# Optimization experiments

Hardware: AMD Instinct MI355X
Metric: run time of the kernel (lower is better)

The kernel has to match this reference:

```python
import jax, jax.numpy as jnp
import numpy as np

D_MODEL = 1024
N_HEAD = 16
D_HEAD = D_MODEL // N_HEAD


def setup_inputs() -> dict:
    key = jax.random.key(0)
    k_x, k_qkv, k_proj = jax.random.split(key, 3)
    B, T = 2, 2048
    x = jax.random.normal(k_x, (B, T, D_MODEL), dtype=jnp.float32)
    # torch Linear weight [out, in]; y = x @ W.T. Scale ~ kaiming-uniform-ish.
    s = 1.0 / np.sqrt(D_MODEL)
    W_qkv = jax.random.uniform(k_qkv, (3 * D_MODEL, D_MODEL), dtype=jnp.float32, minval=-s, maxval=s)
    W_proj = jax.random.uniform(k_proj, (D_MODEL, D_MODEL), dtype=jnp.float32, minval=-s, maxval=s)
    return {"x": x, "W_qkv": W_qkv, "W_proj": W_proj}


def reference(x, W_qkv, W_proj):
    B, T, C = x.shape
    qkv = jnp.einsum('btc,oc->bto', x, W_qkv)  # [B,T,3C]
    q, k, v = jnp.split(qkv, 3, axis=-1)
    # [B,T,C] -> [B,H,T,Dh]
    def heads(t):
        return t.reshape(B, T, N_HEAD, D_HEAD).transpose(0, 2, 1, 3)
    q, k, v = heads(q), heads(k), heads(v)
    scale = 1.0 / np.sqrt(D_HEAD)
    scores = jnp.einsum('bhqd,bhkd->bhqk', q, k) * scale  # [B,H,T,T]
    causal = jnp.tril(jnp.ones((T, T), dtype=bool))
    scores = jnp.where(causal, scores, jnp.finfo(scores.dtype).min)
    attn = jax.nn.softmax(scores, axis=-1)
    y = jnp.einsum('bhqk,bhkd->bhqd', attn, v)  # [B,H,T,Dh]
    y = y.transpose(0, 2, 1, 3).reshape(B, T, C)
    return jnp.einsum('btc,oc->bto', y, W_proj)
```

## Files before the change

kernel.cpp:

```cpp
#include <hip/hip_runtime.h>

typedef unsigned short u16;
typedef float f32x4 __attribute__((ext_vector_type(4)));
typedef __bf16 bf16x8 __attribute__((ext_vector_type(8)));
typedef unsigned int u32x4 __attribute__((ext_vector_type(4)));
typedef u16 u16x4 __attribute__((ext_vector_type(4)));
typedef u16 u16x8 __attribute__((ext_vector_type(8)));

static __device__ __forceinline__ u16 f2bf(float f) {
  union { __bf16 h; u16 u; } c;
  c.h = (__bf16)f;
  return c.u;
}

static __device__ __forceinline__ void gload_lds16(const void* g, void* l) {
  __builtin_amdgcn_global_load_lds(
      (const __attribute__((address_space(1))) unsigned int*)g,
      (__attribute__((address_space(3))) unsigned int*)l, 16, 0, 0);
}

__global__ __launch_bounds__(256) void cvt3_f32_bf16(const float* __restrict__ a,
                                                     const float* __restrict__ bb,
                                                     const float* __restrict__ cc,
                                                     u16* __restrict__ out,
                                                     int n1, int n2, int n3) {
  int i = blockIdx.x * 256 + threadIdx.x;
  const float* src;
  int j = i;
  if (i < n1) { src = a; }
  else if (i < n1 + n2) { src = bb; j = i - n1; }
  else { src = cc; j = i - n1 - n2; if (j >= n3) return; }
  f32x4 v = *((const f32x4*)src + j);
  u16x4 o;
  o[0] = f2bf(v[0]); o[1] = f2bf(v[1]); o[2] = f2bf(v[2]); o[3] = f2bf(v[3]);
  *((u16x4*)out + i) = o;
}

template<int OUT_BF16, int FUSE_VT>
__global__ __launch_bounds__(256) void gemm_nt(const u16* __restrict__ A,
                                               const u16* __restrict__ B,
                                               void* __restrict__ Cp,
                                               u16* __restrict__ vt,
                                               int M, int N, int K, int gy) {
  __shared__ __align__(16) u16 lA[128 * 64];
  __shared__ __align__(16) u16 lB[128 * 64];
  const int tid = threadIdx.x;
  const int lane = tid & 63;
  const int wave = tid >> 6;
  const int wm = wave >> 1, wn = wave & 1;
  const int l15 = lane & 15, lg = lane >> 4;

  const int bid = blockIdx.x;
  const int xcd = bid & 7, s = bid >> 3;
  const int pnx = (N >> 7) >> 3;
  const int bm = (s % gy) * 128;
  const int bn = (xcd * pnx + s / gy) * 128;

  f32x4 acc[4][4];
#pragma unroll
  for (int i = 0; i < 4; ++i)
#pragma unroll
    for (int j = 0; j < 4; ++j) acc[i][j] = (f32x4){0.f, 0.f, 0.f, 0.f};

  const u16* Ag[4];
  const u16* Bg[4];
#pragma unroll
  for (int it = 0; it < 4; ++it) {
    const int ss = it * 256 + tid;
    const int row = ss >> 3, g = ss & 7;
    const int gsw = g ^ (row & 7);
    Ag[it] = A + (size_t)(bm + row) * K + gsw * 8;
    Bg[it] = B + (size_t)(bn + row) * K + gsw * 8;
  }

  for (int k0 = 0; k0 < K; k0 += 64) {
#pragma unroll
    for (int it = 0; it < 4; ++it) {
      gload_lds16(Ag[it] + k0, (u16*)lA + (size_t)(it * 256 + tid) * 8);
      gload_lds16(Bg[it] + k0, (u16*)lB + (size_t)(it * 256 + tid) * 8);
    }
    __syncthreads();
#pragma unroll
    for (int kk = 0; kk < 2; ++kk) {
      bf16x8 af[4], bfv[4];
#pragma unroll
      for (int mf = 0; mf < 4; ++mf) {
        const int row = wm * 64 + mf * 16 + l15;
        af[mf] = *(const bf16x8*)((const char*)lA + row * 128 +
                                  ((kk * 64 + lg * 16) ^ ((row & 7) << 4)));
      }
#pragma unroll
      for (int nf = 0; nf < 4; ++nf) {
        const int row = wn * 64 + nf * 16 + l15;
        bfv[nf] = *(const bf16x8*)((const char*)lB + row * 128 +
                                   ((kk * 64 + lg * 16) ^ ((row & 7) << 4)));
      }
#pragma unroll
      for (int mf = 0; mf < 4; ++mf)
#pragma unroll
        for (int nf = 0; nf < 4; ++nf)
          acc[mf][nf] = __builtin_amdgcn_mfma_f32_16x16x32_bf16(af[mf], bfv[nf], acc[mf][nf], 0, 0, 0);
    }
    __syncthreads();
  }

  if (FUSE_VT && bn >= 2048) {
#pragma unroll
    for (int mf = 0; mf < 4; ++mf) {
      const int row0 = bm + wm * 64 + mf * 16 + lg * 4;
      const int b = row0 >> 11, t0 = row0 & 2047;
#pragma unroll
      for (int nf = 0; nf < 4; ++nf) {
        const int colv = bn - 2048 + wn * 64 + nf * 16 + l15;
        const int h = colv >> 6, d = colv & 63;
        u16x4 pk;
        pk[0] = f2bf(acc[mf][nf][0]); pk[1] = f2bf(acc[mf][nf][1]);
        pk[2] = f2bf(acc[mf][nf][2]); pk[3] = f2bf(acc[mf][nf][3]);
        *(u16x4*)&vt[((size_t)((b * 16 + h) * 64 + d)) * 2048 + t0] = pk;
      }
    }
  } else {
#pragma unroll
    for (int mf = 0; mf < 4; ++mf) {
#pragma unroll
      for (int r = 0; r < 4; ++r) {
        const int row = bm + wm * 64 + mf * 16 + lg * 4 + r;
#pragma unroll
        for (int nf = 0; nf < 4; ++nf) {
          const int col = bn + wn * 64 + nf * 16 + l15;
          const float v = acc[mf][nf][r];
          if (OUT_BF16) ((u16*)Cp)[(size_t)row * N + col] = f2bf(v);
          else          ((float*)Cp)[(size_t)row * N + col] = v;
        }
      }
    }
  }
}

__global__ __launch_bounds__(256) void attn_fwd(const u16* __restrict__ qkv,
                                                const u16* __restrict__ vt,
                                                u16* __restrict__ y) {
  constexpr int T = 2048, C = 1024, C3 = 3072, D = 64, NQ = 32;
  __shared__ __align__(16) u16 lK[2][64 * 64];
  __shared__ __align__(16) u16 lV[3][64 * 64];
  __shared__ __align__(16) u16 lP[4 * 16 * 64];
  const int tid = threadIdx.x, lane = tid & 63, w = tid >> 6;
  const int l15 = lane & 15, lg = lane >> 4;

  const int bid = blockIdx.x;
  const int xcd = bid & 7, slot = bid >> 3;
  const int bh = xcd * 4 + (slot >> 4);
  const int pi = slot & 15;
  const int b = bh >> 4, h = bh & 15;

  const int r0 = tid >> 3, off0 = (tid & 7) * 8;
  const int r1 = (tid + 256) >> 3;
  const int sb0 = (off0 * 2) ^ ((r0 & 7) << 4);
  const int sb1 = (off0 * 2) ^ ((r1 & 7) << 4);
  const u16* Kbase = qkv + (size_t)b * T * C3 + C + h * D;
  const u16* Vbase = vt + (size_t)bh * D * T;

  const float qscale = 0.125f * 1.44269504088896f;

#pragma unroll 1
  for (int qi = 0; qi < 2; ++qi) {
    const int qt = (qi == 0) ? pi : (NQ - 1 - pi);
    const int q0 = qt * 64;

    const size_t qoff = ((size_t)b * T + q0 + w * 16 + l15) * C3 + h * D;
    const bf16x8 aq0 = *(const bf16x8*)&qkv[qoff + lg * 8];
    const bf16x8 aq1 = *(const bf16x8*)&qkv[qoff + 32 + lg * 8];

    float m = -1.0e30f, l = 0.f;
    f32x4 o_acc[4];
#pragma unroll
    for (int nf = 0; nf < 4; ++nf) o_acc[nf] = (f32x4){0.f, 0.f, 0.f, 0.f};

    u32x4 rk0 = *(const u32x4*)(Kbase + (size_t)r0 * C3 + off0);
    u32x4 rk1 = *(const u32x4*)(Kbase + (size_t)r1 * C3 + off0);
    u32x4 rv0 = *(const u32x4*)(Vbase + (size_t)r0 * T + off0);
    u32x4 rv1 = *(const u32x4*)(Vbase + (size_t)r1 * T + off0);
    __syncthreads();
    *(u32x4*)&lK[0][(r0 * 128 + sb0) >> 1] = rk0;
    *(u32x4*)&lK[0][(r1 * 128 + sb1) >> 1] = rk1;
    *(u32x4*)&lV[0][(r0 * 128 + sb0) >> 1] = rv0;
    *(u32x4*)&lV[0][(r1 * 128 + sb1) >> 1] = rv1;
    if (qt >= 1) {
      rk0 = *(const u32x4*)(Kbase + (size_t)(64 + r0) * C3 + off0);
      rk1 = *(const u32x4*)(Kbase + (size_t)(64 + r1) * C3 + off0);
      rv0 = *(const u32x4*)(Vbase + (size_t)r0 * T + 64 + off0);
      rv1 = *(const u32x4*)(Vbase + (size_t)r1 * T + 64 + off0);
    }

    int vcur = 0;
    for (int i = 0; i <= qt + 1; ++i) {
      const int vnext = (vcur == 2) ? 0 : vcur + 1;
      const int vprev = (vcur == 0) ? 2 : vcur - 1;
      __syncthreads();
      const int wr = i + 1;
      if (wr <= qt) {
        *(u32x4*)&lK[wr & 1][(r0 * 128 + sb0) >> 1] = rk0;
        *(u32x4*)&lK[wr & 1][(r1 * 128 + sb1) >> 1] = rk1;
        *(u32x4*)&lV[vnext][(r0 * 128 + sb0) >> 1] = rv0;
        *(u32x4*)&lV[vnext][(r1 * 128 + sb1) >> 1] = rv1;
        if (wr + 1 <= qt) {
          const int kn = (wr + 1) * 64;
          rk0 = *(const u32x4*)(Kbase + (size_t)(kn + r0) * C3 + off0);
          rk1 = *(const u32x4*)(Kbase + (size_t)(kn + r1) * C3 + off0);
          rv0 = *(const u32x4*)(Vbase + (size_t)r0 * T + kn + off0);
          rv1 = *(const u32x4*)(Vbase + (size_t)r1 * T + kn + off0);
        }
      }

      f32x4 s[4];
      if (i <= qt) {
        const u16* Kc = lK[i & 1];
#pragma unroll
        for (int nf = 0; nf < 4; ++nf) s[nf] = (f32x4){0.f, 0.f, 0.f, 0.f};
        __builtin_amdgcn_s_setprio(1);
#pragma unroll
        for (int nf = 0; nf < 4; ++nf) {
          const int row = nf * 16 + l15;
          const int x = (row & 7) << 4;
          bf16x8 bk0 = *(const bf16x8*)&Kc[(row * 128 + ((lg * 16) ^ x)) >> 1];
          bf16x8 bk1 = *(const bf16x8*)&Kc[(row * 128 + ((64 + lg * 16) ^ x)) >> 1];
          s[nf] = __builtin_amdgcn_mfma_f32_16x16x32_bf16(bk0, aq0, s[nf], 0, 0, 0);
          s[nf] = __builtin_amdgcn_mfma_f32_16x16x32_bf16(bk1, aq1, s[nf], 0, 0, 0);
        }
        __builtin_amdgcn_s_setprio(0);
      }

      if (i >= 1) {
        const u16* Vc = lV[vprev];
        __builtin_amdgcn_s_setprio(1);
#pragma unroll
        for (int sj = 0; sj < 2; ++sj) {
          bf16x8 ap = *(const bf16x8*)&lP[(w * 2048 + l15 * 128 + ((sj * 64 + lg * 16) ^ ((l15 & 7) << 4))) >> 1];
#pragma unroll
          for (int nf = 0; nf < 4; ++nf) {
            const int d = nf * 16 + l15;
            bf16x8 bv = *(const bf16x8*)&Vc[(d * 128 + ((sj * 64 + lg * 16) ^ ((d & 7) << 4))) >> 1];
            o_acc[nf] = __builtin_amdgcn_mfma_f32_16x16x32_bf16(ap, bv, o_acc[nf], 0, 0, 0);
          }
        }
        __builtin_amdgcn_s_setprio(0);
      }

      if (i <= qt) {
#pragma unroll
        for (int nf = 0; nf < 4; ++nf) {
#pragma unroll
          for (int r = 0; r < 4; ++r) {
            float v = s[nf][r] * qscale;
            if (i == qt) {
              if (nf * 16 + lg * 4 + r > w * 16 + l15) v = -1.0e30f;
            }
            s[nf][r] = v;
          }
        }

        float t0a = fmaxf(fmaxf(s[0][0], s[0][1]), fmaxf(s[0][2], s[0][3]));
        float t1a = fmaxf(fmaxf(s[1][0], s[1][1]), fmaxf(s[1][2], s[1][3]));
        float t2a = fmaxf(fmaxf(s[2][0], s[2][1]), fmaxf(s[2][2], s[2][3]));
        float t3a = fmaxf(fmaxf(s[3][0], s[3][1]), fmaxf(s[3][2], s[3][3]));
        float pmax = fmaxf(fmaxf(t0a, t1a), fmaxf(t2a, t3a));
        pmax = fmaxf(pmax, __shfl_xor(pmax, 16));
        pmax = fmaxf(pmax, __shfl_xor(pmax, 32));

        if (!__all(pmax <= m)) {
          const float mnew = fmaxf(m, pmax);
          const float fct = __builtin_amdgcn_exp2f(m - mnew);
          m = mnew;
          l *= fct;
#pragma unroll
          for (int r = 0; r < 4; ++r) {
            const float fr = __shfl(fct, lg * 4 + r);
#pragma unroll
            for (int nf = 0; nf < 4; ++nf) o_acc[nf][r] *= fr;
          }
        }

        float p[4][4];
#pragma unroll
        for (int nf = 0; nf < 4; ++nf)
#pragma unroll
          for (int r = 0; r < 4; ++r) p[nf][r] = __builtin_amdgcn_exp2f(s[nf][r] - m);
        float s0a = (p[0][0] + p[0][1]) + (p[0][2] + p[0][3]);
        float s1a = (p[1][0] + p[1][1]) + (p[1][2] + p[1][3]);
        float s2a = (p[2][0] + p[2][1]) + (p[2][2] + p[2][3]);
        float s3a = (p[3][0] + p[3][1]) + (p[3][2] + p[3][3]);
        float psum = (s0a + s1a) + (s2a + s3a);
        psum += __shfl_xor(psum, 16);
        psum += __shfl_xor(psum, 32);
        l += psum;

#pragma unroll
        for (int nf = 0; nf < 4; ++nf) {
          u16x4 pk;
          pk[0] = f2bf(p[nf][0]); pk[1] = f2bf(p[nf][1]);
          pk[2] = f2bf(p[nf][2]); pk[3] = f2bf(p[nf][3]);
          *(u16x4*)&lP[(w * 2048 + l15 * 128 + ((nf * 32 + lg * 8) ^ ((l15 & 7) << 4))) >> 1] = pk;
        }
      }

      vcur = vnext;
    }

#pragma unroll
    for (int r = 0; r < 4; ++r) {
      const float li = __builtin_amdgcn_rcpf(__shfl(l, lg * 4 + r));
      const int row = q0 + w * 16 + lg * 4 + r;
#pragma unroll
      for (int nf = 0; nf < 4; ++nf) {
        const int col = h * D + nf * 16 + l15;
        y[((size_t)b * T + row) * C + col] = f2bf(o_acc[nf][r] * li);
      }
    }
  }
}

extern "C" void kernel_launch(void* const* d_in, const int* in_sizes, int n_in,
                              void* d_out, int out_size, void* d_ws, size_t ws_size,
                              hipStream_t stream) {
  const float* x = (const float*)d_in[0];
  const float* Wqkv = (const float*)d_in[1];
  const float* Wproj = (const float*)d_in[2];
  float* out = (float*)d_out;

  constexpr int B = 2, T = 2048, C = 1024, C3 = 3072, H = 16, D = 64;
  constexpr int M = B * T;

  u16* xb = (u16*)d_ws;
  u16* wqkvb = xb + (size_t)M * C;
  u16* wprojb = wqkvb + (size_t)C3 * C;
  u16* qkvb = wprojb + (size_t)C * C;
  u16* vtb = qkvb + (size_t)M * C3;
  u16* yb = vtb + (size_t)M * C;

  constexpr int n1 = (M * C) / 4, n2 = (C3 * C) / 4, n3 = (C * C) / 4;
  cvt3_f32_bf16<<<dim3((n1 + n2 + n3 + 255) / 256), 256, 0, stream>>>(
      x, Wqkv, Wproj, xb, n1, n2, n3);

  gemm_nt<1, 1><<<dim3((C3 / 128) * (M / 128)), 256, 0, stream>>>(
      xb, wqkvb, qkvb, vtb, M, C3, C, M / 128);
  attn_fwd<<<dim3(512), 256, 0, stream>>>(qkvb, vtb, yb);
  gemm_nt<0, 0><<<dim3((C / 128) * (M / 128)), 256, 0, stream>>>(
      yb, wprojb, out, nullptr, M, C, C, M / 128);
}
```

Before: 114.5 us.

## Add 256x256 tiled QKV GEMM with direct-to-LDS loads and simplify attention pipeline

Adds a new gemm256 kernel with 256x256 output tiles, 512 threads and double-buffered global_load_lds staging, and uses it for the QKV projection instead of the 128x128 gemm_nt. The larger tile is meant to raise arithmetic intensity and cut global traffic. The attention kernel also drops its skewed software pipeline, where P·V lagged one K tile behind Q·K, in favour of a simple loop that computes QK, softmax and PV on the same tile with double buffers. This saves one V buffer but removes the overlap between the two matmuls. The grid is now 192 blocks, which may underfill 256 CUs.

```diff
diff --git a/kernel.cpp b/kernel.cpp
--- a/kernel.cpp
+++ b/kernel.cpp
@@ -137,12 +137,172 @@
   }
 }
 
+template<int OUT_BF16, int FUSE_VT>
+__global__ __launch_bounds__(512, 2) void gemm256(const u16* __restrict__ A,
+                                                  const u16* __restrict__ B,
+                                                  void* __restrict__ Cp,
+                                                  u16* __restrict__ vt,
+                                                  int M, int N, int K) {
+  __shared__ __align__(16) u16 shm[65536];
+  const int tid = threadIdx.x;
+  const int lane = tid & 63, wave = tid >> 6;
+  const int wm = wave >> 2, wn = wave & 3;
+  const int l15 = lane & 15, lg = lane >> 4;
+
+  const int bid = blockIdx.x;
+  const int g = (bid & 7) * ((int)gridDim.x >> 3) + (bid >> 3);
+  const int bm = (g & 15) * 256;
+  const int bn = (g >> 4) * 256;
+
+  size_t srcA[2][2], srcB[2][2];
+  int lo[2];
+#pragma unroll
+  for (int i = 0; i < 2; ++i) {
+    const int flat = i * 512 + tid;
+    const int row = flat >> 3, gg = flat & 7;
+    const int gsw = gg ^ (row & 7);
+    lo[i] = flat * 16;
+#pragma unroll
+    for (int half = 0; half < 2; ++half) {
+      srcA[i][half] = (size_t)(bm + half * 128 + row) * K + gsw * 8;
+      srcB[i][half] = (size_t)(bn + half * 128 + row) * K + gsw * 8;
+    }
+  }
+
+#define STAGE_A(buf, half, kt)                                                     \
+  do {                                                                             \
+    gload_lds16(A + srcA[0][half] + (size_t)(kt) * 64,                             \
+                (char*)shm + (buf) * 65536 + (half) * 16384 + lo[0]);              \
+    gload_lds16(A + srcA[1][half] + (size_t)(kt) * 64,                             \
+                (char*)shm + (buf) * 65536 + (half) * 16384 + lo[1]);              \
+  } while (0)
+#define STAGE_B(buf, half, kt)                                                     \
+  do {                                                                             \
+    gload_lds16(B + srcB[0][half] + (size_t)(kt) * 64,                             \
+                (char*)shm + (buf) * 65536 + 32768 + (half) * 16384 + lo[0]);      \
+    gload_lds16(B + srcB[1][half] + (size_t)(kt) * 64,                             \
+                (char*)shm + (buf) * 65536 + 32768 + (half) * 16384 + lo[1]);      \
+  } while (0)
+
+  f32x4 acc[8][4];
+#pragma unroll
+  for (int i = 0; i < 8; ++i)
+#pragma unroll
+    for (int j = 0; j < 4; ++j) acc[i][j] = (f32x4){0.f, 0.f, 0.f, 0.f};
+
+  STAGE_A(0, 0, 0); STAGE_A(0, 1, 0);
+  STAGE_B(0, 0, 0); STAGE_B(0, 1, 0);
+  STAGE_B(1, 0, 1); STAGE_B(1, 1, 1);
+  asm volatile("s_waitcnt vmcnt(4)" ::: "memory");
+  __builtin_amdgcn_s_barrier();
+  __builtin_amdgcn_sched_barrier(0);
+
+  const int NT2 = K / 128;
+#pragma unroll 1
+  for (int t = 0; t < NT2; ++t) {
+    const int k0 = 2 * t, k1 = 2 * t + 1;
+    const bool more = (t < NT2 - 1);
+
+#pragma unroll
+    for (int grp = 0; grp < 2; ++grp) {
+      const char* Ab = (char*)shm + grp * 65536;
+      const char* Bb = Ab + 32768;
+      bf16x8 bB[4][2];
+#pragma unroll
+      for (int j = 0; j < 4; ++j) {
+        if (j == 0) {
+#pragma unroll
+          for (int nn = 0; nn < 4; ++nn) {
+            const int r = wn * 64 + nn * 16 + l15;
+            const int x = (r & 7) << 4;
+            bB[nn][0] = *(const bf16x8*)(Bb + r * 128 + ((lg * 16) ^ x));
+            bB[nn][1] = *(const bf16x8*)(Bb + r * 128 + ((64 + lg * 16) ^ x));
+          }
+        }
+        bf16x8 af[2][2];
+#pragma unroll
+        for (int mm = 0; mm < 2; ++mm) {
+          const int r = wm * 128 + (2 * j + mm) * 16 + l15;
+          const int x = (r & 7) << 4;
+          af[mm][0] = *(const bf16x8*)(Ab + r * 128 + ((lg * 16) ^ x));
+          af[mm][1] = *(const bf16x8*)(Ab + r * 128 + ((64 + lg * 16) ^ x));
+        }
+        if (grp == 0) {
+          if (j == 0) { STAGE_A(1, 0, k1); }
+          if (j == 1) { STAGE_A(1, 1, k1); if (more) STAGE_B(0, 0, k0 + 2); }
+          if (j == 2) { if (more) STAGE_B(0, 1, k0 + 2); }
+        } else {
+          if (j == 0) { if (more) STAGE_A(0, 0, k0 + 2); }
+          if (j == 1) { if (more) { STAGE_A(0, 1, k0 + 2); STAGE_B(1, 0, k1 + 2); } }
+          if (j == 2) { if (more) STAGE_B(1, 1, k1 + 2); }
+        }
+        __builtin_amdgcn_s_barrier();
+        __builtin_amdgcn_s_setprio(1);
+#pragma unroll
+        for (int mm = 0; mm < 2; ++mm)
+#pragma unroll
+          for (int nn = 0; nn < 4; ++nn) {
+            acc[2 * j + mm][nn] = __builtin_amdgcn_mfma_f32_16x16x32_bf16(
+                af[mm][0], bB[nn][0], acc[2 * j + mm][nn], 0, 0, 0);
+            acc[2 * j + mm][nn] = __builtin_amdgcn_mfma_f32_16x16x32_bf16(
+                af[mm][1], bB[nn][1], acc[2 * j + mm][nn], 0, 0, 0);
+          }
+        __builtin_amdgcn_s_setprio(0);
+        if (j == 3) {
+          if (grp == 0) {
+            if (more) asm volatile("s_waitcnt vmcnt(4)" ::: "memory");
+            else      asm volatile("s_waitcnt vmcnt(0)" ::: "memory");
+          } else if (more) {
+            asm volatile("s_waitcnt vmcnt(4)" ::: "memory");
+          }
+        }
+        __builtin_amdgcn_s_barrier();
+        if (j == 3) __builtin_amdgcn_sched_barrier(0);
+      }
+    }
+  }
+#undef STAGE_A
+#undef STAGE_B
+
+  if (FUSE_VT && bn >= 2048) {
+#pragma unroll
+    for (int m = 0; m < 8; ++m) {
+      const int row0 = bm + wm * 128 + m * 16 + lg * 4;
+      const int b = row0 >> 11, t0 = row0 & 2047;
+#pragma unroll
+      for (int nn = 0; nn < 4; ++nn) {
+        const int colv = bn - 2048 + wn * 64 + nn * 16 + l15;
+        const int h = colv >> 6, d = colv & 63;
+        u16x4 pk;
+        pk[0] = f2bf(acc[m][nn][0]); pk[1] = f2bf(acc[m][nn][1]);
+        pk[2] = f2bf(acc[m][nn][2]); pk[3] = f2bf(acc[m][nn][3]);
+        *(u16x4*)&vt[((size_t)((b * 16 + h) * 64 + d)) * 2048 + t0] = pk;
+      }
+    }
+  } else {
+#pragma unroll
+    for (int m = 0; m < 8; ++m) {
+#pragma unroll
+      for (int r = 0; r < 4; ++r) {
+        const int row = bm + wm * 128 + m * 16 + lg * 4 + r;
+#pragma unroll
+        for (int nn = 0; nn < 4; ++nn) {
+          const int col = bn + wn * 64 + nn * 16 + l15;
+          const float v = acc[m][nn][r];
+          if (OUT_BF16) ((u16*)Cp)[(size_t)row * N + col] = f2bf(v);
+          else          ((float*)Cp)[(size_t)row * N + col] = v;
+        }
+      }
+    }
+  }
+}
+
 __global__ __launch_bounds__(256) void attn_fwd(const u16* __restrict__ qkv,
                                                 const u16* __restrict__ vt,
                                                 u16* __restrict__ y) {
   constexpr int T = 2048, C = 1024, C3 = 3072, D = 64, NQ = 32;
   __shared__ __align__(16) u16 lK[2][64 * 64];
-  __shared__ __align__(16) u16 lV[3][64 * 64];
+  __shared__ __align__(16) u16 lV[2][64 * 64];
   __shared__ __align__(16) u16 lP[4 * 16 * 64];
   const int tid = threadIdx.x, lane = tid & 63, w = tid >> 6;
   const int l15 = lane & 15, lg = lane >> 4;
@@ -185,125 +345,114 @@
     *(u32x4*)&lK[0][(r1 * 128 + sb1) >> 1] = rk1;
     *(u32x4*)&lV[0][(r0 * 128 + sb0) >> 1] = rv0;
     *(u32x4*)&lV[0][(r1 * 128 + sb1) >> 1] = rv1;
-    if (qt >= 1) {
+    if (qt > 0) {
       rk0 = *(const u32x4*)(Kbase + (size_t)(64 + r0) * C3 + off0);
       rk1 = *(const u32x4*)(Kbase + (size_t)(64 + r1) * C3 + off0);
       rv0 = *(const u32x4*)(Vbase + (size_t)r0 * T + 64 + off0);
       rv1 = *(const u32x4*)(Vbase + (size_t)r1 * T + 64 + off0);
     }
 
-    int vcur = 0;
-    for (int i = 0; i <= qt + 1; ++i) {
-      const int vnext = (vcur == 2) ? 0 : vcur + 1;
-      const int vprev = (vcur == 0) ? 2 : vcur - 1;
+    for (int kt = 0; kt <= qt; ++kt) {
+      const int cur = kt & 1;
       __syncthreads();
-      const int wr = i + 1;
-      if (wr <= qt) {
-        *(u32x4*)&lK[wr & 1][(r0 * 128 + sb0) >> 1] = rk0;
-        *(u32x4*)&lK[wr & 1][(r1 * 128 + sb1) >> 1] = rk1;
-        *(u32x4*)&lV[vnext][(r0 * 128 + sb0) >> 1] = rv0;
-        *(u32x4*)&lV[vnext][(r1 * 128 + sb1) >> 1] = rv1;
-        if (wr + 1 <= qt) {
-          const int kn = (wr + 1) * 64;
+      if (kt < qt) {
+        *(u32x4*)&lK[cur ^ 1][(r0 * 128 + sb0) >> 1] = rk0;
+        *(u32x4*)&lK[cur ^ 1][(r1 * 128 + sb1) >> 1] = rk1;
+        *(u32x4*)&lV[cur ^ 1][(r0 * 128 + sb0) >> 1] = rv0;
+        *(u32x4*)&lV[cur ^ 1][(r1 * 128 + sb1) >> 1] = rv1;
+        if (kt + 1 < qt) {
+          const int kn = (kt + 2) * 64;
           rk0 = *(const u32x4*)(Kbase + (size_t)(kn + r0) * C3 + off0);
           rk1 = *(const u32x4*)(Kbase + (size_t)(kn + r1) * C3 + off0);
           rv0 = *(const u32x4*)(Vbase + (size_t)r0 * T + kn + off0);
           rv1 = *(const u32x4*)(Vbase + (size_t)r1 * T + kn + off0);
         }
       }
+      const u16* Kc = lK[cur];
+      const u16* Vc = lV[cur];
 
       f32x4 s[4];
-      if (i <= qt) {
-        const u16* Kc = lK[i & 1];
-#pragma unroll
-        for (int nf = 0; nf < 4; ++nf) s[nf] = (f32x4){0.f, 0.f, 0.f, 0.f};
-        __builtin_amdgcn_s_setprio(1);
+#pragma unroll
+      for (int nf = 0; nf < 4; ++nf) s[nf] = (f32x4){0.f, 0.f, 0.f, 0.f};
+      __builtin_amdgcn_s_setprio(1);
+#pragma unroll
+      for (int nf = 0; nf < 4; ++nf) {
+        const int row = nf * 16 + l15;
+        const int x = (row & 7) << 4;
+        bf16x8 bk0 = *(const bf16x8*)&Kc[(row * 128 + ((lg * 16) ^ x)) >> 1];
+        bf16x8 bk1 = *(const bf16x8*)&Kc[(row * 128 + ((64 + lg * 16) ^ x)) >> 1];
+        s[nf] = __builtin_amdgcn_mfma_f32_16x16x32_bf16(bk0, aq0, s[nf], 0, 0, 0);
+        s[nf] = __builtin_amdgcn_mfma_f32_16x16x32_bf16(bk1, aq1, s[nf], 0, 0, 0);
+      }
+      __builtin_amdgcn_s_setprio(0);
+
+#pragma unroll
+      for (int nf = 0; nf < 4; ++nf) {
+#pragma unroll
+        for (int r = 0; r < 4; ++r) {
+          float v = s[nf][r] * qscale;
+          if (kt == qt) {
+            if (nf * 16 + lg * 4 + r > w * 16 + l15) v = -1.0e30f;
+          }
+          s[nf][r] = v;
+        }
+      }
+
+      float t0a = fmaxf(fmaxf(s[0][0], s[0][1]), fmaxf(s[0][2], s[0][3]));
+      float t1a = fmaxf(fmaxf(s[1][0], s[1][1]), fmaxf(s[1][2], s[1][3]));
+      float t2a = fmaxf(fmaxf(s[2][0], s[2][1]), fmaxf(s[2][2], s[2][3]));
+      float t3a = fmaxf(fmaxf(s[3][0], s[3][1]), fmaxf(s[3][2], s[3][3]));
+      float pmax = fmaxf(fmaxf(t0a, t1a), fmaxf(t2a, t3a));
+      pmax = fmaxf(pmax, __shfl_xor(pmax, 16));
+      pmax = fmaxf(pmax, __shfl_xor(pmax, 32));
+
+      if (!__all(pmax <= m)) {
+        const float mnew = fmaxf(m, pmax);
+        const float fct = __builtin_amdgcn_exp2f(m - mnew);
+        m = mnew;
+        l *= fct;
+#pragma unroll
+        for (int r = 0; r < 4; ++r) {
+          const float fr = __shfl(fct, lg * 4 + r);
+#pragma unroll
+          for (int nf = 0; nf < 4; ++nf) o_acc[nf][r] *= fr;
+        }
+      }
+
+      float p[4][4];
+#pragma unroll
+      for (int nf = 0; nf < 4; ++nf)
+#pragma unroll
+        for (int r = 0; r < 4; ++r) p[nf][r] = __builtin_amdgcn_exp2f(s[nf][r] - m);
+      float s0a = (p[0][0] + p[0][1]) + (p[0][2] + p[0][3]);
+      float s1a = (p[1][0] + p[1][1]) + (p[1][2] + p[1][3]);
+      float s2a = (p[2][0] + p[2][1]) + (p[2][2] + p[2][3]);
+      float s3a = (p[3][0] + p[3][1]) + (p[3][2] + p[3][3]);
+      float psum = (s0a + s1a) + (s2a + s3a);
+      psum += __shfl_xor(psum, 16);
+      psum += __shfl_xor(psum, 32);
+      l += psum;
+
+#pragma unroll
+      for (int nf = 0; nf < 4; ++nf) {
+        u16x4 pk;
+        pk[0] = f2bf(p[nf][0]); pk[1] = f2bf(p[nf][1]);
+        pk[2] = f2bf(p[nf][2]); pk[3] = f2bf(p[nf][3]);
+        *(u16x4*)&lP[(w * 2048 + l15 * 128 + ((nf * 32 + lg * 8) ^ ((l15 & 7) << 4))) >> 1] = pk;
+      }
+
+      __builtin_amdgcn_s_setprio(1);
+#pragma unroll
+      for (int sj = 0; sj < 2; ++sj) {
+        bf16x8 ap = *(const bf16x8*)&lP[(w * 2048 + l15 * 128 + ((sj * 64 + lg * 16) ^ ((l15 & 7) << 4))) >> 1];
 #pragma unroll
         for (int nf = 0; nf < 4; ++nf) {
-          const int row = nf * 16 + l15;
-          const int x = (row & 7) << 4;
-          bf16x8 bk0 = *(const bf16x8*)&Kc[(row * 128 + ((lg * 16) ^ x)) >> 1];
-          bf16x8 bk1 = *(const bf16x8*)&Kc[(row * 128 + ((64 + lg * 16) ^ x)) >> 1];
-          s[nf] = __builtin_amdgcn_mfma_f32_16x16x32_bf16(bk0, aq0, s[nf], 0, 0, 0);
-          s[nf] = __builtin_amdgcn_mfma_f32_16x16x32_bf16(bk1, aq1, s[nf], 0, 0, 0);
-        }
-        __builtin_amdgcn_s_setprio(0);
-      }
-
-      if (i >= 1) {
-        const u16* Vc = lV[vprev];
-        __builtin_amdgcn_s_setprio(1);
-#pragma unroll
-        for (int sj = 0; sj < 2; ++sj) {
-          bf16x8 ap = *(const bf16x8*)&lP[(w * 2048 + l15 * 128 + ((sj * 64 + lg * 16) ^ ((l15 & 7) << 4))) >> 1];
-#pragma unroll
-          for (int nf = 0; nf < 4; ++nf) {
-            const int d = nf * 16 + l15;
-            bf16x8 bv = *(const bf16x8*)&Vc[(d * 128 + ((sj * 64 + lg * 16) ^ ((d & 7) << 4))) >> 1];
-            o_acc[nf] = __builtin_amdgcn_mfma_f32_16x16x32_bf16(ap, bv, o_acc[nf], 0, 0, 0);
-          }
-        }
-        __builtin_amdgcn_s_setprio(0);
-      }
-
-      if (i <= qt) {
-#pragma unroll
-        for (int nf = 0; nf < 4; ++nf) {
-#pragma unroll
-          for (int r = 0; r < 4; ++r) {
-            float v = s[nf][r] * qscale;
-            if (i == qt) {
-              if (nf * 16 + lg * 4 + r > w * 16 + l15) v = -1.0e30f;
-            }
-            s[nf][r] = v;
-          }
-        }
-
-        float t0a = fmaxf(fmaxf(s[0][0], s[0][1]), fmaxf(s[0][2], s[0][3]));
-        float t1a = fmaxf(fmaxf(s[1][0], s[1][1]), fmaxf(s[1][2], s[1][3]));
-        float t2a = fmaxf(fmaxf(s[2][0], s[2][1]), fmaxf(s[2][2], s[2][3]));
-        float t3a = fmaxf(fmaxf(s[3][0], s[3][1]), fmaxf(s[3][2], s[3][3]));
-        float pmax = fmaxf(fmaxf(t0a, t1a), fmaxf(t2a, t3a));
-        pmax = fmaxf(pmax, __shfl_xor(pmax, 16));
-        pmax = fmaxf(pmax, __shfl_xor(pmax, 32));
-
-        if (!__all(pmax <= m)) {
-          const float mnew = fmaxf(m, pmax);
-          const float fct = __builtin_amdgcn_exp2f(m - mnew);
-          m = mnew;
-          l *= fct;
-#pragma unroll
-          for (int r = 0; r < 4; ++r) {
-            const float fr = __shfl(fct, lg * 4 + r);
-#pragma unroll
-            for (int nf = 0; nf < 4; ++nf) o_acc[nf][r] *= fr;
-          }
-        }
-
-        float p[4][4];
-#pragma unroll
-        for (int nf = 0; nf < 4; ++nf)
-#pragma unroll
-          for (int r = 0; r < 4; ++r) p[nf][r] = __builtin_amdgcn_exp2f(s[nf][r] - m);
-        float s0a = (p[0][0] + p[0][1]) + (p[0][2] + p[0][3]);
-        float s1a = (p[1][0] + p[1][1]) + (p[1][2] + p[1][3]);
-        float s2a = (p[2][0] + p[2][1]) + (p[2][2] + p[2][3]);
-        float s3a = (p[3][0] + p[3][1]) + (p[3][2] + p[3][3]);
-        float psum = (s0a + s1a) + (s2a + s3a);
-        psum += __shfl_xor(psum, 16);
-        psum += __shfl_xor(psum, 32);
-        l += psum;
-
-#pragma unroll
-        for (int nf = 0; nf < 4; ++nf) {
-          u16x4 pk;
-          pk[0] = f2bf(p[nf][0]); pk[1] = f2bf(p[nf][1]);
-          pk[2] = f2bf(p[nf][2]); pk[3] = f2bf(p[nf][3]);
-          *(u16x4*)&lP[(w * 2048 + l15 * 128 + ((nf * 32 + lg * 8) ^ ((l15 & 7) << 4))) >> 1] = pk;
-        }
-      }
-
-      vcur = vnext;
+          const int d = nf * 16 + l15;
+          bf16x8 bv = *(const bf16x8*)&Vc[(d * 128 + ((sj * 64 + lg * 16) ^ ((d & 7) << 4))) >> 1];
+          o_acc[nf] = __builtin_amdgcn_mfma_f32_16x16x32_bf16(ap, bv, o_acc[nf], 0, 0, 0);
+        }
+      }
+      __builtin_amdgcn_s_setprio(0);
     }
 
 #pragma unroll
@@ -341,8 +490,8 @@
   cvt3_f32_bf16<<<dim3((n1 + n2 + n3 + 255) / 256), 256, 0, stream>>>(
       x, Wqkv, Wproj, xb, n1, n2, n3);
 
-  gemm_nt<1, 1><<<dim3((C3 / 128) * (M / 128)), 256, 0, stream>>>(
-      xb, wqkvb, qkvb, vtb, M, C3, C, M / 128);
+  gemm256<1, 1><<<dim3((C3 / 256) * (M / 256)), 512, 0, stream>>>(
+      xb, wqkvb, qkvb, vtb, M, C3, C);
   attn_fwd<<<dim3(512), 256, 0, stream>>>(qkvb, vtb, yb);
   gemm_nt<0, 0><<<dim3((C / 128) * (M / 128)), 256, 0, stream>>>(
       yb, wprojb, out, nullptr, M, C, C, M / 128);
```

Measured after the change: 116.9 us. 2.1% more time.

## Use 128-row query tiles with 8 waves and drop the skewed PV pipeline

Applied to the files above, without the earlier changes.

The attention kernel now runs 512-thread blocks (8 waves) over 128-query tiles, so each K/V tile loaded into LDS is shared by twice as many query rows. Each thread loads one row chunk instead of two. The one-iteration skew between QK and PV, which needed a triple-buffered V, is replaced by a straight per-tile QK→softmax→PV sequence over double-buffered K/V. This cuts global and LDS load traffic per query, but halves the number of blocks to 256 and serialises softmax and PV inside each iteration. It also spends more work on masked diagonal tiles, since two 64-wide diagonal tiles are now masked per query tile.

```diff
diff --git a/kernel.cpp b/kernel.cpp
--- a/kernel.cpp
+++ b/kernel.cpp
@@ -137,37 +137,38 @@
   }
 }
 
-__global__ __launch_bounds__(256) void attn_fwd(const u16* __restrict__ qkv,
+__global__ __launch_bounds__(512) void attn_fwd(const u16* __restrict__ qkv,
                                                 const u16* __restrict__ vt,
                                                 u16* __restrict__ y) {
-  constexpr int T = 2048, C = 1024, C3 = 3072, D = 64, NQ = 32;
+  constexpr int T = 2048, C = 1024, C3 = 3072, D = 64;
   __shared__ __align__(16) u16 lK[2][64 * 64];
-  __shared__ __align__(16) u16 lV[3][64 * 64];
-  __shared__ __align__(16) u16 lP[4 * 16 * 64];
+  __shared__ __align__(16) u16 lV[2][64 * 64];
+  __shared__ __align__(16) u16 lP[8 * 16 * 64];
   const int tid = threadIdx.x, lane = tid & 63, w = tid >> 6;
   const int l15 = lane & 15, lg = lane >> 4;
 
   const int bid = blockIdx.x;
   const int xcd = bid & 7, slot = bid >> 3;
-  const int bh = xcd * 4 + (slot >> 4);
-  const int pi = slot & 15;
+  const int bh = xcd * 4 + (slot >> 3);
+  const int pi = slot & 7;
   const int b = bh >> 4, h = bh & 15;
 
   const int r0 = tid >> 3, off0 = (tid & 7) * 8;
-  const int r1 = (tid + 256) >> 3;
   const int sb0 = (off0 * 2) ^ ((r0 & 7) << 4);
-  const int sb1 = (off0 * 2) ^ ((r1 & 7) << 4);
   const u16* Kbase = qkv + (size_t)b * T * C3 + C + h * D;
   const u16* Vbase = vt + (size_t)bh * D * T;
+  char* lPb = (char*)lP + w * 2048;
 
   const float qscale = 0.125f * 1.44269504088896f;
 
 #pragma unroll 1
   for (int qi = 0; qi < 2; ++qi) {
-    const int qt = (qi == 0) ? pi : (NQ - 1 - pi);
-    const int q0 = qt * 64;
-
-    const size_t qoff = ((size_t)b * T + q0 + w * 16 + l15) * C3 + h * D;
+    const int qt = (qi == 0) ? pi : (15 - pi);
+    const int q0 = qt * 128;
+    const int nkt = 2 * qt + 2;
+    const int qrow = q0 + w * 16 + l15;
+
+    const size_t qoff = ((size_t)b * T + qrow) * C3 + h * D;
     const bf16x8 aq0 = *(const bf16x8*)&qkv[qoff + lg * 8];
     const bf16x8 aq1 = *(const bf16x8*)&qkv[qoff + 32 + lg * 8];
 
@@ -177,133 +178,117 @@
     for (int nf = 0; nf < 4; ++nf) o_acc[nf] = (f32x4){0.f, 0.f, 0.f, 0.f};
 
     u32x4 rk0 = *(const u32x4*)(Kbase + (size_t)r0 * C3 + off0);
-    u32x4 rk1 = *(const u32x4*)(Kbase + (size_t)r1 * C3 + off0);
     u32x4 rv0 = *(const u32x4*)(Vbase + (size_t)r0 * T + off0);
-    u32x4 rv1 = *(const u32x4*)(Vbase + (size_t)r1 * T + off0);
     __syncthreads();
     *(u32x4*)&lK[0][(r0 * 128 + sb0) >> 1] = rk0;
-    *(u32x4*)&lK[0][(r1 * 128 + sb1) >> 1] = rk1;
     *(u32x4*)&lV[0][(r0 * 128 + sb0) >> 1] = rv0;
-    *(u32x4*)&lV[0][(r1 * 128 + sb1) >> 1] = rv1;
-    if (qt >= 1) {
+    if (nkt > 1) {
       rk0 = *(const u32x4*)(Kbase + (size_t)(64 + r0) * C3 + off0);
-      rk1 = *(const u32x4*)(Kbase + (size_t)(64 + r1) * C3 + off0);
       rv0 = *(const u32x4*)(Vbase + (size_t)r0 * T + 64 + off0);
-      rv1 = *(const u32x4*)(Vbase + (size_t)r1 * T + 64 + off0);
-    }
-
-    int vcur = 0;
-    for (int i = 0; i <= qt + 1; ++i) {
-      const int vnext = (vcur == 2) ? 0 : vcur + 1;
-      const int vprev = (vcur == 0) ? 2 : vcur - 1;
+    }
+
+    for (int kt = 0; kt < nkt; ++kt) {
+      const int cur = kt & 1;
       __syncthreads();
-      const int wr = i + 1;
-      if (wr <= qt) {
-        *(u32x4*)&lK[wr & 1][(r0 * 128 + sb0) >> 1] = rk0;
-        *(u32x4*)&lK[wr & 1][(r1 * 128 + sb1) >> 1] = rk1;
-        *(u32x4*)&lV[vnext][(r0 * 128 + sb0) >> 1] = rv0;
-        *(u32x4*)&lV[vnext][(r1 * 128 + sb1) >> 1] = rv1;
-        if (wr + 1 <= qt) {
-          const int kn = (wr + 1) * 64;
+      if (kt < nkt - 1) {
+        *(u32x4*)&lK[cur ^ 1][(r0 * 128 + sb0) >> 1] = rk0;
+        *(u32x4*)&lV[cur ^ 1][(r0 * 128 + sb0) >> 1] = rv0;
+        if (kt + 1 < nkt - 1) {
+          const int kn = (kt + 2) * 64;
           rk0 = *(const u32x4*)(Kbase + (size_t)(kn + r0) * C3 + off0);
-          rk1 = *(const u32x4*)(Kbase + (size_t)(kn + r1) * C3 + off0);
           rv0 = *(const u32x4*)(Vbase + (size_t)r0 * T + kn + off0);
-          rv1 = *(const u32x4*)(Vbase + (size_t)r1 * T + kn + off0);
         }
       }
+      const u16* Kc = lK[cur];
+      const u16* Vc = lV[cur];
 
       f32x4 s[4];
-      if (i <= qt) {
-        const u16* Kc = lK[i & 1];
-#pragma unroll
-        for (int nf = 0; nf < 4; ++nf) s[nf] = (f32x4){0.f, 0.f, 0.f, 0.f};
-        __builtin_amdgcn_s_setprio(1);
-#pragma unroll
-        for (int nf = 0; nf < 4; ++nf) {
-          const int row = nf * 16 + l15;
-          const int x = (row & 7) << 4;
-          bf16x8 bk0 = *(const bf16x8*)&Kc[(row * 128 + ((lg * 16) ^ x)) >> 1];
-          bf16x8 bk1 = *(const bf16x8*)&Kc[(row * 128 + ((64 + lg * 16) ^ x)) >> 1];
-          s[nf] = __builtin_amdgcn_mfma_f32_16x16x32_bf16(bk0, aq0, s[nf], 0, 0, 0);
-          s[nf] = __builtin_amdgcn_mfma_f32_16x16x32_bf16(bk1, aq1, s[nf], 0, 0, 0);
-        }
-        __builtin_amdgcn_s_setprio(0);
-      }
-
-      if (i >= 1) {
-        const u16* Vc = lV[vprev];
-        __builtin_amdgcn_s_setprio(1);
-#pragma unroll
-        for (int sj = 0; sj < 2; ++sj) {
-          bf16x8 ap = *(const bf16x8*)&lP[(w * 2048 + l15 * 128 + ((sj * 64 + lg * 16) ^ ((l15 & 7) << 4))) >> 1];
-#pragma unroll
-          for (int nf = 0; nf < 4; ++nf) {
-            const int d = nf * 16 + l15;
-            bf16x8 bv = *(const bf16x8*)&Vc[(d * 128 + ((sj * 64 + lg * 16) ^ ((d & 7) << 4))) >> 1];
-            o_acc[nf] = __builtin_amdgcn_mfma_f32_16x16x32_bf16(ap, bv, o_acc[nf], 0, 0, 0);
-          }
-        }
-        __builtin_amdgcn_s_setprio(0);
-      }
-
-      if (i <= qt) {
-#pragma unroll
-        for (int nf = 0; nf < 4; ++nf) {
+#pragma unroll
+      for (int nf = 0; nf < 4; ++nf) s[nf] = (f32x4){0.f, 0.f, 0.f, 0.f};
+      __builtin_amdgcn_s_setprio(1);
+#pragma unroll
+      for (int nf = 0; nf < 4; ++nf) {
+        const int row = nf * 16 + l15;
+        const int x = (row & 7) << 4;
+        bf16x8 bk0 = *(const bf16x8*)&Kc[(row * 128 + ((lg * 16) ^ x)) >> 1];
+        bf16x8 bk1 = *(const bf16x8*)&Kc[(row * 128 + ((64 + lg * 16) ^ x)) >> 1];
+        s[nf] = __builtin_amdgcn_mfma_f32_16x16x32_bf16(bk0, aq0, s[nf], 0, 0, 0);
+        s[nf] = __builtin_amdgcn_mfma_f32_16x16x32_bf16(bk1, aq1, s[nf], 0, 0, 0);
+      }
+      __builtin_amdgcn_s_setprio(0);
+
+      if (kt >= 2 * qt) {
+        const int kb = kt * 64;
+#pragma unroll
+        for (int nf = 0; nf < 4; ++nf)
 #pragma unroll
           for (int r = 0; r < 4; ++r) {
             float v = s[nf][r] * qscale;
-            if (i == qt) {
-              if (nf * 16 + lg * 4 + r > w * 16 + l15) v = -1.0e30f;
-            }
+            if (kb + nf * 16 + lg * 4 + r > qrow) v = -1.0e30f;
             s[nf][r] = v;
           }
+      } else {
+#pragma unroll
+        for (int nf = 0; nf < 4; ++nf)
+#pragma unroll
+          for (int r = 0; r < 4; ++r) s[nf][r] *= qscale;
+      }
+
+      float t0a = fmaxf(fmaxf(s[0][0], s[0][1]), fmaxf(s[0][2], s[0][3]));
+      float t1a = fmaxf(fmaxf(s[1][0], s[1][1]), fmaxf(s[1][2], s[1][3]));
+      float t2a = fmaxf(fmaxf(s[2][0], s[2][1]), fmaxf(s[2][2], s[2][3]));
+      float t3a = fmaxf(fmaxf(s[3][0], s[3][1]), fmaxf(s[3][2], s[3][3]));
+      float pmax = fmaxf(fmaxf(t0a, t1a), fmaxf(t2a, t3a));
+      pmax = fmaxf(pmax, __shfl_xor(pmax, 16));
+      pmax = fmaxf(pmax, __shfl_xor(pmax, 32));
+
+      if (!__all(pmax <= m)) {
+        const float mnew = fmaxf(m, pmax);
+        const float fct = __builtin_amdgcn_exp2f(m - mnew);
+        m = mnew;
+        l *= fct;
+#pragma unroll
+        for (int r = 0; r < 4; ++r) {
+          const float fr = __shfl(fct, lg * 4 + r);
+#pragma unroll
+          for (int nf = 0; nf < 4; ++nf) o_acc[nf][r] *= fr;
         }
-
-        float t0a = fmaxf(fmaxf(s[0][0], s[0][1]), fmaxf(s[0][2], s[0][3]));
-        float t1a = fmaxf(fmaxf(s[1][0], s[1][1]), fmaxf(s[1][2], s[1][3]));
-        float t2a = fmaxf(fmaxf(s[2][0], s[2][1]), fmaxf(s[2][2], s[2][3]));
-        float t3a = fmaxf(fmaxf(s[3][0], s[3][1]), fmaxf(s[3][2], s[3][3]));
-        float pmax = fmaxf(fmaxf(t0a, t1a), fmaxf(t2a, t3a));
-        pmax = fmaxf(pmax, __shfl_xor(pmax, 16));
-        pmax = fmaxf(pmax, __shfl_xor(pmax, 32));
-
-        if (!__all(pmax <= m)) {
-          const float mnew = fmaxf(m, pmax);
-          const float fct = __builtin_amdgcn_exp2f(m - mnew);
-          m = mnew;
-          l *= fct;
-#pragma unroll
-          for (int r = 0; r < 4; ++r) {
-            const float fr = __shfl(fct, lg * 4 + r);
-#pragma unroll
-            for (int nf = 0; nf < 4; ++nf) o_acc[nf][r] *= fr;
-          }
+      }
+
+      float p[4][4];
+#pragma unroll
+      for (int nf = 0; nf < 4; ++nf)
+#pragma unroll
+        for (int r = 0; r < 4; ++r) p[nf][r] = __builtin_amdgcn_exp2f(s[nf][r] - m);
+      float s0a = (p[0][0] + p[0][1]) + (p[0][2] + p[0][3]);
+      float s1a = (p[1][0] + p[1][1]) + (p[1][2] + p[1][3]);
+      float s2a = (p[2][0] + p[2][1]) + (p[2][2] + p[2][3]);
+      float s3a = (p[3][0] + p[3][1]) + (p[3][2] + p[3][3]);
+      float psum = (s0a + s1a) + (s2a + s3a);
+      psum += __shfl_xor(psum, 16);
+      psum += __shfl_xor(psum, 32);
+      l += psum;
+
+#pragma unroll
+      for (int nf = 0; nf < 4; ++nf) {
+        u16x4 pk;
+        pk[0] = f2bf(p[nf][0]); pk[1] = f2bf(p[nf][1]);
+        pk[2] = f2bf(p[nf][2]); pk[3] = f2bf(p[nf][3]);
+        *(u16x4*)(lPb + l15 * 128 + ((nf * 32 + lg * 8) ^ ((l15 & 7) << 4))) = pk;
+      }
+
+      __builtin_amdgcn_s_setprio(1);
+#pragma unroll
+      for (int sj = 0; sj < 2; ++sj) {
+        bf16x8 ap = *(const bf16x8*)(lPb + l15 * 128 + ((sj * 64 + lg * 16) ^ ((l15 & 7) << 4)));
+#pragma unroll
+        for (int nf = 0; nf < 4; ++nf) {
+          const int d = nf * 16 + l15;
+          bf16x8 bv = *(const bf16x8*)&Vc[(d * 128 + ((sj * 64 + lg * 16) ^ ((d & 7) << 4))) >> 1];
+          o_acc[nf] = __builtin_amdgcn_mfma_f32_16x16x32_bf16(ap, bv, o_acc[nf], 0, 0, 0);
         }
-
-        float p[4][4];
-#pragma unroll
-        for (int nf = 0; nf < 4; ++nf)
-#pragma unroll
-          for (int r = 0; r < 4; ++r) p[nf][r] = __builtin_amdgcn_exp2f(s[nf][r] - m);
-        float s0a = (p[0][0] + p[0][1]) + (p[0][2] + p[0][3]);
-        float s1a = (p[1][0] + p[1][1]) + (p[1][2] + p[1][3]);
-        float s2a = (p[2][0] + p[2][1]) + (p[2][2] + p[2][3]);
-        float s3a = (p[3][0] + p[3][1]) + (p[3][2] + p[3][3]);
-        float psum = (s0a + s1a) + (s2a + s3a);
-        psum += __shfl_xor(psum, 16);
-        psum += __shfl_xor(psum, 32);
-        l += psum;
-
-#pragma unroll
-        for (int nf = 0; nf < 4; ++nf) {
-          u16x4 pk;
-          pk[0] = f2bf(p[nf][0]); pk[1] = f2bf(p[nf][1]);
-          pk[2] = f2bf(p[nf][2]); pk[3] = f2bf(p[nf][3]);
-          *(u16x4*)&lP[(w * 2048 + l15 * 128 + ((nf * 32 + lg * 8) ^ ((l15 & 7) << 4))) >> 1] = pk;
-        }
-      }
-
-      vcur = vnext;
+      }
+      __builtin_amdgcn_s_setprio(0);
     }
 
 #pragma unroll
@@ -343,7 +328,7 @@
 
   gemm_nt<1, 1><<<dim3((C3 / 128) * (M / 128)), 256, 0, stream>>>(
       xb, wqkvb, qkvb, vtb, M, C3, C, M / 128);
-  attn_fwd<<<dim3(512), 256, 0, stream>>>(qkvb, vtb, yb);
+  attn_fwd<<<dim3(256), 512, 0, stream>>>(qkvb, vtb, yb);
   gemm_nt<0, 0><<<dim3((C / 128) * (M / 128)), 256, 0, stream>>>(
       yb, wprojb, out, nullptr, M, C, C, M / 128);
 }
```

Measured after the change: 112.8 us. Within noise of the previous version (-1.4%).
